# Performance work log

Measured on AMD Instinct MI355X. Metric: run time of the kernel, lower is better.

The kernel has to match this reference:

```python
import jax, jax.numpy as jnp
import numpy as np

N_E = 8192
E_DIM = 256
BETA = 0.25


def setup_inputs() -> dict:
    key = jax.random.key(0)
    k_z, k_w = jax.random.split(key)
    z = jax.random.normal(k_z, (32, E_DIM, 32, 32), dtype=jnp.float32)
    # nn.Embedding weight init: uniform(-1/n_e, 1/n_e)
    W = jax.random.uniform(k_w, (N_E, E_DIM), dtype=jnp.float32,
                           minval=-1.0 / N_E, maxval=1.0 / N_E)
    return {"z": z, "W": W}


def reference(z, W):
    B, C, H, Wd = z.shape
    beta = jnp.float32(BETA)
    z_nhwc = jnp.transpose(z, (0, 2, 3, 1))          # (B,H,W,C)
    zf = z_nhwc.reshape(-1, C)                       # (N,C)
    # squared-distance matrix (N, n_e)
    d = (jnp.sum(zf * zf, axis=1, keepdims=True)
         + jnp.sum(W * W, axis=1)
         - 2.0 * jnp.matmul(zf, W.T))
    idx = jnp.argmin(d, axis=1)                      # (N,)
    # one-hot @ W == gather
    z_q = W[idx].reshape(z_nhwc.shape)               # (B,H,W,C)
    loss = (jnp.mean((jax.lax.stop_gradient(z_q) - z_nhwc) ** 2)
            + beta * jnp.mean((z_q - jax.lax.stop_gradient(z_nhwc)) ** 2))
    # straight-through estimator
    z_q = z_nhwc + jax.lax.stop_gradient(z_q - z_nhwc)
    # codebook usage perplexity
    n = idx.shape[0]
    e_mean = jnp.zeros((N_E,), jnp.float32).at[idx].add(1.0) / n
    perplexity = jnp.exp(-jnp.sum(e_mean * jnp.log(e_mean + 1e-10)))
    z_q = jnp.transpose(z_q, (0, 3, 1, 2))           # back to (B,C,H,W)
    index = idx.reshape(B, H, Wd)
    return z_q, loss, index, perplexity
```

## Files before the change

kernel.cpp:

```cpp
#include <hip/hip_runtime.h>
#include <float.h>
#include <math.h>

#define OUT_LOSS 8388608
#define OUT_IDX  8388609
#define OUT_PERP 8421377

#define WS_ZH    0ull
#define WS_ZL    16777216ull
#define WS_ZT    0ull
#define WS_WH    33554432ull
#define WS_S     37748736ull
#define WS_B     37879808ull
#define WS_MAXW  37912576ull
#define WS_IDX   37912640ull
#define WS_HIST  38043712ull
#define WS_CAND  38076480ull
#define WS_FULL  38469696ull
#define WS_FKEY  38600768ull
#define WS_CNT   38862912ull
#define WS_LOSS  38862920ull
#define WS_WL    38866944ull

typedef short v8s __attribute__((ext_vector_type(8)));
typedef float v4f __attribute__((ext_vector_type(4)));

__device__ __forceinline__ unsigned short bf16rne(float f) {
  unsigned u = __float_as_uint(f);
  return (unsigned short)((u + 0x7FFFu + ((u >> 16) & 1u)) >> 16);
}
__device__ __forceinline__ float bf16tof(unsigned short h) {
  return __uint_as_float(((unsigned)h) << 16);
}

__device__ __forceinline__ void gl_lds16(const void* g, void* l) {
  __builtin_amdgcn_global_load_lds(
      (const __attribute__((address_space(1))) unsigned int*)g,
      (__attribute__((address_space(3))) unsigned int*)l, 16, 0, 0);
}

__global__ void k_zero(int* __restrict__ hist, unsigned long long* __restrict__ fkey,
                       int* __restrict__ cnt, double* __restrict__ loss,
                       unsigned* __restrict__ maxw) {
  const int i = blockIdx.x * 256 + threadIdx.x;
  if (i < 8192) hist[i] = 0;
  else if (i < 40960) fkey[i - 8192] = ~0ull;
  else if (i == 40960) cnt[0] = 0;
  else if (i == 40961) cnt[1] = 0;
  else if (i == 40962) *loss = 0.0;
  else if (i == 40963) *maxw = 0u;
}

__global__ __launch_bounds__(256) void k_split(const float* __restrict__ W,
                                               unsigned short* __restrict__ Wh,
                                               unsigned short* __restrict__ Wl) {
  const int u = blockIdx.x * 256 + threadIdx.x;
  const int kc = u >> 15, grp = (u >> 6) & 511, q = (u >> 4) & 3, col = u & 15;
  const int j = grp * 16 + col, k0 = kc * 32 + q * 8;
  const float4 w0 = *(const float4*)(W + (size_t)j * 256 + k0);
  const float4 w1 = *(const float4*)(W + (size_t)j * 256 + k0 + 4);
  const float wv[8] = {w0.x, w0.y, w0.z, w0.w, w1.x, w1.y, w1.z, w1.w};
  unsigned short h[8] __attribute__((aligned(16)));
  unsigned short l[8] __attribute__((aligned(16)));
#pragma unroll
  for (int i = 0; i < 8; ++i) {
    h[i] = bf16rne(wv[i]);
    l[i] = bf16rne(__fsub_rn(wv[i], bf16tof(h[i])));
  }
  *(uint4*)(Wh + (size_t)u * 8) = *(const uint4*)h;
  *(uint4*)(Wl + (size_t)u * 8) = *(const uint4*)l;
}

__global__ __launch_bounds__(256) void k_splitz(const float* __restrict__ z,
    unsigned short* __restrict__ Zh, unsigned short* __restrict__ Zl) {
  const int gt = blockIdx.x * 256 + threadIdx.x;
  const int kc = gt >> 15;
  const int n  = gt & 32767;
  const int b = n >> 10, p = n & 1023;
  const float* zp = z + (size_t)b * 262144 + (size_t)(kc * 32) * 1024 + p;
  unsigned short hh[32] __attribute__((aligned(16)));
  unsigned short ll[32] __attribute__((aligned(16)));
#pragma unroll
  for (int i = 0; i < 32; ++i) {
    const float v = zp[(size_t)i * 1024];
    const unsigned short h = bf16rne(v);
    hh[i] = h;
    ll[i] = bf16rne(__fsub_rn(v, bf16tof(h)));
  }
  const size_t o = (size_t)kc * 1048576 + (size_t)(n >> 4) * 512 + (size_t)(n & 15) * 8;
#pragma unroll
  for (int q = 0; q < 4; ++q) *(uint4*)(Zh + o + q * 128) = *(const uint4*)(hh + q * 8);
#pragma unroll
  for (int q = 0; q < 4; ++q) *(uint4*)(Zl + o + q * 128) = *(const uint4*)(ll + q * 8);
}

__global__ __launch_bounds__(256) void k_zt(const float* __restrict__ z,
                                            float* __restrict__ zT) {
  const int gt = blockIdx.x * 256 + threadIdx.x;
  const int kc = gt >> 15;
  const int n  = gt & 32767;
  const int b = n >> 10, p = n & 1023;
  const float* zp = z + (size_t)b * 262144 + (size_t)(kc * 32) * 1024 + p;
  float v[32] __attribute__((aligned(16)));
#pragma unroll
  for (int i = 0; i < 32; ++i) v[i] = zp[(size_t)i * 1024];
  float* dst = zT + (size_t)n * 256 + kc * 32;
#pragma unroll
  for (int j = 0; j < 8; ++j) *(float4*)(dst + j * 4) = *(const float4*)(v + j * 4);
}

__device__ __forceinline__ float np_sumsq256(const float* __restrict__ base,
                                             const int stride) {
  float h[2];
#pragma unroll
  for (int half = 0; half < 2; ++half) {
    const float* a = base + (size_t)(half * 128) * stride;
    float r[8];
#pragma unroll
    for (int k = 0; k < 8; ++k) { const float v = a[(size_t)k * stride]; r[k] = __fmul_rn(v, v); }
    for (int i = 8; i < 128; i += 8) {
#pragma unroll
      for (int k = 0; k < 8; ++k) {
        const float v = a[(size_t)(i + k) * stride];
        r[k] = __fadd_rn(r[k], __fmul_rn(v, v));
      }
    }
    h[half] = __fadd_rn(
        __fadd_rn(__fadd_rn(r[0], r[1]), __fadd_rn(r[2], r[3])),
        __fadd_rn(__fadd_rn(r[4], r[5]), __fadd_rn(r[6], r[7])));
  }
  return __fadd_rn(h[0], h[1]);
}

__global__ __launch_bounds__(256) void k_sz(const float* __restrict__ z,
                                            float* __restrict__ S) {
  const int n = blockIdx.x * 256 + threadIdx.x;
  S[n] = np_sumsq256(z + (size_t)(n >> 10) * 262144 + (n & 1023), 1024);
}

__global__ __launch_bounds__(256) void k_wsq(const float* __restrict__ W,
                                             float* __restrict__ B,
                                             unsigned* __restrict__ maxw) {
  const int j = blockIdx.x * 256 + threadIdx.x;
  const float b = np_sumsq256(W + (size_t)j * 256, 1);
  B[j] = b;
  atomicMax(maxw, __float_as_uint(b));
}

__device__ __forceinline__ void merge5(float& a1, int& ai1, float& a2, int& ai2,
                                       float& a3, float b1, int bi1, float b2,
                                       int bi2, float b3) {
  const bool t1 = (b1 < a1) || (b1 == a1 && bi1 < ai1);
  const float w2v = t1 ? b2 : a2; const int w2i = t1 ? bi2 : ai2;
  const float w3v = t1 ? b3 : a3;
  const float l1v = t1 ? a1 : b1; const int l1i = t1 ? ai1 : bi1;
  const float l2v = t1 ? a2 : b2;
  const float n1v = t1 ? b1 : a1; const int n1i = t1 ? bi1 : ai1;
  const bool t2 = (w2v < l1v) || (w2v == l1v && w2i < l1i);
  a1 = n1v; ai1 = n1i;
  a2 = t2 ? w2v : l1v; ai2 = t2 ? w2i : l1i;
  a3 = t2 ? fminf(w3v, l1v) : fminf(w2v, l2v);
}

#define AH_OFF   0
#define AL_OFF   32768
#define B0_OFF   65536
#define B1_OFF   73728
#define SC_OFF   0
#define SMEM_SZ  81920
__global__ __launch_bounds__(256, 2) void k_main(
    const unsigned short* __restrict__ Zh, const unsigned short* __restrict__ Zl,
    const unsigned short* __restrict__ Wh, const unsigned short* __restrict__ Wl,
    const float* __restrict__ S, const float* __restrict__ B,
    const unsigned* __restrict__ maxw, int* __restrict__ idxb,
    int* __restrict__ cand, int* __restrict__ full, int* __restrict__ cnt) {
  extern __shared__ __align__(16) char smem[];
  const int t = threadIdx.x;
  const int w = t >> 6, lane = t & 63, col = lane & 15, q = lane >> 4;
  const int phalf = w >> 1, strip = w & 1;
  const int n0 = blockIdx.x << 6;

  float spx[8];
#pragma unroll
  for (int s = 0; s < 8; ++s)
    spx[s] = S[n0 + phalf * 32 + (s >> 2) * 16 + q * 4 + (s & 3)];

  {
#pragma unroll
    for (int c = 0; c < 2; ++c) {
      const int kc = w * 2 + c;
      const size_t ab = (size_t)kc * 1048576 + (size_t)(n0 >> 4) * 512 + (size_t)lane * 8;
#pragma unroll
      for (int g = 0; g < 4; ++g) {
        gl_lds16(Zh + ab + (size_t)g * 512, smem + AH_OFF + kc * 4096 + g * 1024);
        gl_lds16(Zl + ab + (size_t)g * 512, smem + AL_OFF + kc * 4096 + g * 1024);
      }
    }
  }
  {
    const size_t bb = (size_t)(w * 2) * 512 + (size_t)lane * 8;
    gl_lds16(Wh + bb,       smem + B0_OFF + (w * 2) * 1024);
    gl_lds16(Wh + bb + 512, smem + B0_OFF + (w * 2 + 1) * 1024);
  }
  v8s bl[4];
  {
    const unsigned short* p = Wl + (size_t)(strip * 4) * 512 + (size_t)lane * 8;
#pragma unroll
    for (int nt = 0; nt < 4; ++nt) bl[nt] = *(const v8s*)(p + nt * 512);
  }
  __syncthreads();

  float m1[8], m2[8], m3[8]; int i1[8], i2[8];
#pragma unroll
  for (int s = 0; s < 8; ++s) {
    m1[s] = FLT_MAX; m2[s] = FLT_MAX; m3[s] = FLT_MAX;
    i1[s] = 0x7fffffff; i2[s] = 0x7fffffff;
  }

  v4f acc[2][4];
#pragma unroll
  for (int pt = 0; pt < 2; ++pt)
#pragma unroll
    for (int nt = 0; nt < 4; ++nt) acc[pt][nt] = (v4f){0.f, 0.f, 0.f, 0.f};

  for (int ct = 0; ct < 64; ++ct) {
#pragma unroll
    for (int kc = 0; kc < 8; ++kc) {
      const int it = ct * 8 + kc;
      if (it < 511) {
        const int nc = it + 1;
        const size_t cb = (size_t)(nc & 7) * 262144 + (size_t)(nc >> 3) * 4096
                        + (size_t)(w * 2) * 512 + (size_t)lane * 8;
        char* nh = smem + ((nc & 1) ? B1_OFF : B0_OFF) + (w * 2) * 1024;
        gl_lds16(Wh + cb,       nh);
        gl_lds16(Wh + cb + 512, nh + 1024);
      }
      const char* bhb = smem + ((it & 1) ? B1_OFF : B0_OFF);
      const int nc2 = (it + 1) & 511;
      const unsigned short* blsrc = Wl + (size_t)(nc2 & 7) * 262144
                                  + (size_t)(nc2 >> 3) * 4096
                                  + (size_t)(strip * 4) * 512 + (size_t)lane * 8;
      v8s ah[2], al[2];
#pragma unroll
      for (int pt = 0; pt < 2; ++pt) {
        const int g = phalf * 2 + pt;
        ah[pt] = *(const v8s*)(smem + AH_OFF + kc * 4096 + g * 1024 + lane * 16);
        al[pt] = *(const v8s*)(smem + AL_OFF + kc * 4096 + g * 1024 + lane * 16);
      }
#pragma unroll
      for (int nt = 0; nt < 4; ++nt) {
        const v8s bh = *(const v8s*)(bhb + (strip * 4 + nt) * 1024 + lane * 16);
        const v8s blv = bl[nt];
#pragma unroll
        for (int pt = 0; pt < 2; ++pt) {
          acc[pt][nt] = __builtin_amdgcn_mfma_f32_16x16x32_bf16(ah[pt], bh, acc[pt][nt], 0, 0, 0);
          acc[pt][nt] = __builtin_amdgcn_mfma_f32_16x16x32_bf16(al[pt], bh, acc[pt][nt], 0, 0, 0);
          acc[pt][nt] = __builtin_amdgcn_mfma_f32_16x16x32_bf16(ah[pt], blv, acc[pt][nt], 0, 0, 0);
        }
        bl[nt] = *(const v8s*)(blsrc + nt * 512);
      }
      __syncthreads();
      if (kc == 7) {
#pragma unroll
        for (int nt = 0; nt < 4; ++nt) {
          const int code = ct * 128 + strip * 64 + nt * 16 + col;
          const float bb = B[code];
#pragma unroll
          for (int pt = 0; pt < 2; ++pt) {
            const v4f a = acc[pt][nt];
#pragma unroll
            for (int r = 0; r < 4; ++r) {
              const int s = pt * 4 + r;
              const float d = __fsub_rn(__fadd_rn(spx[s], bb), __fmul_rn(2.f, a[r]));
              const bool c1 = (d < m1[s]);
              const bool c2 = (d < m2[s]);
              const bool c3 = (d < m3[s]);
              m3[s] = c2 ? m2[s] : (c3 ? d : m3[s]);
              m2[s] = c1 ? m1[s] : (c2 ? d : m2[s]);
              i2[s] = c1 ? i1[s] : (c2 ? code : i2[s]);
              m1[s] = c1 ? d : m1[s];
              i1[s] = c1 ? code : i1[s];
            }
          }
#pragma unroll
          for (int pt = 0; pt < 2; ++pt) acc[pt][nt] = (v4f){0.f, 0.f, 0.f, 0.f};
        }
      }
    }
  }

#pragma unroll
  for (int s = 0; s < 8; ++s) {
    for (int msk = 1; msk < 16; msk <<= 1) {
      const float b1 = __shfl_xor(m1[s], msk, 16);
      const int  bi1 = __shfl_xor(i1[s], msk, 16);
      const float b2 = __shfl_xor(m2[s], msk, 16);
      const int  bi2 = __shfl_xor(i2[s], msk, 16);
      const float b3 = __shfl_xor(m3[s], msk, 16);
      merge5(m1[s], i1[s], m2[s], i2[s], m3[s], b1, bi1, b2, bi2, b3);
    }
  }
  __syncthreads();
  float* sc = (float*)(smem + SC_OFF);
  if (col == 0) {
#pragma unroll
    for (int s = 0; s < 8; ++s) {
      const int px = phalf * 32 + (s >> 2) * 16 + q * 4 + (s & 3);
      const int base = (px * 2 + strip) * 5;
      sc[base]     = m1[s];
      sc[base + 1] = __int_as_float(i1[s]);
      sc[base + 2] = m2[s];
      sc[base + 3] = __int_as_float(i2[s]);
      sc[base + 4] = m3[s];
    }
  }
  __syncthreads();
  if (t < 64) {
    const int base0 = t * 10;
    float A1 = sc[base0], A2 = sc[base0 + 2], A3 = sc[base0 + 4];
    int AI1 = __float_as_int(sc[base0 + 1]), AI2 = __float_as_int(sc[base0 + 3]);
    {
      const int base = base0 + 5;
      merge5(A1, AI1, A2, AI2, A3, sc[base], __float_as_int(sc[base + 1]),
             sc[base + 2], __float_as_int(sc[base + 3]), sc[base + 4]);
    }
    const int n = n0 + t;
    idxb[n] = AI1;
    const float nw = sqrtf(S[n]) * sqrtf(__uint_as_float(*maxw));
    const float win = 2.0f * (1.52587890625e-05f * nw + 1e-6f)
                    + 2.0f * ldexpf(1.0f, ilogbf(fmaxf(A1, 1e-30f)) - 23);
    if (A2 <= A1 + win) {
      if (A3 <= A1 + win) {
        const int p = atomicAdd(&cnt[1], 1);
        full[p] = n;
      } else {
        const int p = atomicAdd(&cnt[0], 1);
        cand[3 * p] = n; cand[3 * p + 1] = AI1; cand[3 * p + 2] = AI2;
      }
    }
  }
}

__global__ __launch_bounds__(256) void k_cand(const float* __restrict__ zT,
    const float* __restrict__ W, const float* __restrict__ S,
    const float* __restrict__ B, const int* __restrict__ cand,
    const int* __restrict__ cnt, int* __restrict__ idxb) {
  const int e = blockIdx.x * 256 + threadIdx.x;
  if (e >= cnt[0]) return;
  const int n = cand[3 * e], ca = cand[3 * e + 1], cb = cand[3 * e + 2];
  const float* zp = zT + (size_t)n * 256;
  const float* wa = W + (size_t)ca * 256;
  const float* wb = W + (size_t)cb * 256;
  float a1 = 0.f, a2 = 0.f;
  for (int c = 0; c < 256; ++c) {
    const float zv = zp[c];
    a1 = __builtin_fmaf(zv, wa[c], a1);
    a2 = __builtin_fmaf(zv, wb[c], a2);
  }
  const float d1 = __fsub_rn(__fadd_rn(S[n], B[ca]), __fmul_rn(2.f, a1));
  const float d2 = __fsub_rn(__fadd_rn(S[n], B[cb]), __fmul_rn(2.f, a2));
  idxb[n] = (d1 < d2) ? ca : ((d2 < d1) ? cb : min(ca, cb));
}

__global__ __launch_bounds__(256) void k_full(const float* __restrict__ zT,
    const float* __restrict__ W, const float* __restrict__ S,
    const float* __restrict__ B, const int* __restrict__ full,
    const int* __restrict__ cnt, unsigned long long* __restrict__ fkey) {
  extern __shared__ __align__(16) char fsm[];
  float* zsf = (float*)fsm;
  float* wt  = (float*)(fsm + 32768);
  float* mv  = (float*)(fsm + 32768 + 32896);
  int*   mi  = (int*)(fsm + 32768 + 32896 + 4224);
  const int t = threadIdx.x;
  const int pg = t & 7, cg = t >> 3;
  const int fN = min(cnt[1], 32768);
  const int units = ((fN + 31) >> 5) << 5;
  for (int e = blockIdx.x; e < units; e += 2048) {
    const int g = e >> 5, tt = e & 31;
    const int c0 = tt << 8;
    __syncthreads();
    {
      const int px = t >> 3, c8 = t & 7;
      const int f = (g << 5) + px;
      const int n = (f < fN) ? full[f] : full[0];
      const float4* src = (const float4*)(zT + (size_t)n * 256 + c8 * 32);
      const int colq = (((px >> 2) ^ c8) << 2) + (px & 3);
#pragma unroll
      for (int j = 0; j < 8; ++j) {
        const float4 v = src[j];
        const int c = c8 * 32 + j * 4;
        zsf[(c    ) * 32 + colq] = v.x;
        zsf[(c + 1) * 32 + colq] = v.y;
        zsf[(c + 2) * 32 + colq] = v.z;
        zsf[(c + 3) * 32 + colq] = v.w;
      }
    }
    float s4[4];
#pragma unroll
    for (int i = 0; i < 4; ++i) {
      const int f = (g << 5) + (pg << 2) + i;
      s4[i] = (f < fN) ? S[full[f]] : 0.f;
    }
    float bm[4]; int bj[4];
#pragma unroll
    for (int i = 0; i < 4; ++i) { bm[i] = FLT_MAX; bj[i] = 0x7fffffff; }
    float acc[4][8];
#pragma unroll
    for (int i = 0; i < 4; ++i)
#pragma unroll
      for (int u = 0; u < 8; ++u) acc[i][u] = 0.f;
    for (int kc = 0; kc < 8; ++kc) {
      const int kb = kc << 5;
      __syncthreads();
#pragma unroll
      for (int p = 0; p < 8; ++p) {
        const int jl = (t >> 3) + (p << 5);
        const float4 wv4 =
            *(const float4*)&W[(size_t)(c0 + jl) * 256 + kb + ((t & 7) << 2)];
        const int k0 = (t & 7) << 2;
        wt[(k0    ) * 257 + jl] = wv4.x;
        wt[(k0 + 1) * 257 + jl] = wv4.y;
        wt[(k0 + 2) * 257 + jl] = wv4.z;
        wt[(k0 + 3) * 257 + jl] = wv4.w;
      }
      __syncthreads();
      const int zq = ((pg ^ kc) & 7) << 2;
      for (int k = 0; k < 32; ++k) {
        const float4 z4 = *(const float4*)&zsf[(kb + k) * 32 + zq];
        const float4 wA = *(const float4*)&wt[k * 257 + (cg << 3)];
        const float4 wB = *(const float4*)&wt[k * 257 + (cg << 3) + 4];
        const float zv[4] = {z4.x, z4.y, z4.z, z4.w};
        const float wv[8] = {wA.x, wA.y, wA.z, wA.w, wB.x, wB.y, wB.z, wB.w};
#pragma unroll
        for (int i = 0; i < 4; ++i)
#pragma unroll
          for (int u = 0; u < 8; ++u)
            acc[i][u] = __builtin_fmaf(zv[i], wv[u], acc[i][u]);
      }
    }
#pragma unroll
    for (int u = 0; u < 8; ++u) {
      const int code = c0 + (cg << 3) + u;
      const float bb = B[code];
#pragma unroll
      for (int i = 0; i < 4; ++i) {
        const float d = __fsub_rn(__fadd_rn(s4[i], bb), __fmul_rn(2.f, acc[i][u]));
        if (d < bm[i]) { bm[i] = d; bj[i] = code; }
      }
    }
    __syncthreads();
#pragma unroll
    for (int i = 0; i < 4; ++i) {
      const int px = (pg << 2) + i;
      mv[px * 33 + cg] = bm[i];
      mi[px * 33 + cg] = bj[i];
    }
    __syncthreads();
    if (t < 32) {
      float m = mv[t * 33]; int j = mi[t * 33];
      for (int c = 1; c < 32; ++c) {
        const float v = mv[t * 33 + c]; const int vi = mi[t * 33 + c];
        if (v < m || (v == m && vi < j)) { m = v; j = vi; }
      }
      const int f = (g << 5) + t;
      if (f < fN) {
        const unsigned long long key =
            (((unsigned long long)__float_as_uint(m)) << 13) | (unsigned)j;
        atomicMin(&fkey[f], key);
      }
    }
  }
}

__global__ __launch_bounds__(256) void k_fullfin(const int* __restrict__ full,
    const int* __restrict__ cnt, const unsigned long long* __restrict__ fkey,
    int* __restrict__ idxb) {
  const int f = blockIdx.x * 256 + threadIdx.x;
  if (f < cnt[1]) idxb[full[f]] = (int)(fkey[f] & 8191ull);
}

__global__ __launch_bounds__(256) void k_zq(const float* __restrict__ z,
    const float* __restrict__ W, const int* __restrict__ idxb,
    float* __restrict__ out, double* __restrict__ loss, int* __restrict__ hist) {
  __shared__ float red[256];
  const int t = threadIdx.x;
  const int tx = t & 63, ty = t >> 6;
  const int n0 = blockIdx.x << 6;
  const int n = n0 + tx;
  const int b = n >> 10;
  const int p = n & 1023;
  const int myidx = idxb[n];
  const float* wrow = W + (size_t)myidx * 256;
  float lsum = 0.f;
#pragma unroll 4
  for (int cc = 0; cc < 64; ++cc) {
    const int c = ty * 64 + cc;
    const float qv = wrow[c];
    const size_t off = (size_t)b * 262144 + (size_t)c * 1024 + p;
    const float zv = z[off];
    const float d = __fsub_rn(qv, zv);
    lsum = __builtin_fmaf(d, d, lsum);
    out[off] = __fadd_rn(zv, d);
  }
  red[t] = lsum;
  __syncthreads();
  for (int o = 128; o > 0; o >>= 1) {
    if (t < o) red[t] += red[t + o];
    __syncthreads();
  }
  if (t == 0) atomicAdd(loss, (double)red[0]);
  if (ty == 0) atomicAdd(&hist[myidx], 1);
  if (ty == 1) out[OUT_IDX + n] = (float)myidx;
}

__global__ void k_final(const int* __restrict__ hist,
                        const double* __restrict__ loss,
                        float* __restrict__ out) {
  __shared__ double sh[256];
  const int t = threadIdx.x;
  double s = 0.0;
  for (int j = t; j < 8192; j += 256) {
    const double e = (double)hist[j] / 32768.0;
    s += e * log(e + 1e-10);
  }
  sh[t] = s;
  __syncthreads();
  for (int off = 128; off > 0; off >>= 1) {
    if (t < off) sh[t] += sh[t + off];
    __syncthreads();
  }
  if (t == 0) {
    out[OUT_PERP] = (float)exp(-sh[0]);
    out[OUT_LOSS] = (float)(1.25 * (*loss) / 8388608.0);
  }
}

extern "C" void kernel_launch(void* const* d_in, const int* in_sizes, int n_in,
                              void* d_out, int out_size, void* d_ws, size_t ws_size,
                              hipStream_t stream) {
  const float* z = (const float*)d_in[0];
  const float* W = (const float*)d_in[1];
  float* out = (float*)d_out;
  char* ws = (char*)d_ws;
  unsigned short* Zh = (unsigned short*)(ws + WS_ZH);
  unsigned short* Zl = (unsigned short*)(ws + WS_ZL);
  unsigned short* Wh = (unsigned short*)(ws + WS_WH);
  unsigned short* Wl = (unsigned short*)(ws + WS_WL);
  float*  zT   = (float*)(ws + WS_ZT);
  float*  S    = (float*)(ws + WS_S);
  float*  B    = (float*)(ws + WS_B);
  unsigned* maxw = (unsigned*)(ws + WS_MAXW);
  int*    idxb = (int*)(ws + WS_IDX);
  int*    hist = (int*)(ws + WS_HIST);
  int*    cand = (int*)(ws + WS_CAND);
  int*    full = (int*)(ws + WS_FULL);
  unsigned long long* fkey = (unsigned long long*)(ws + WS_FKEY);
  int*    cnt  = (int*)(ws + WS_CNT);
  double* loss = (double*)(ws + WS_LOSS);

  hipLaunchKernelGGL(k_zero,    dim3(161),  dim3(256), 0, stream, hist, fkey, cnt, loss, maxw);
  hipLaunchKernelGGL(k_split,   dim3(1024), dim3(256), 0, stream, W, Wh, Wl);
  hipLaunchKernelGGL(k_splitz,  dim3(1024), dim3(256), 0, stream, z, Zh, Zl);
  hipLaunchKernelGGL(k_sz,      dim3(128),  dim3(256), 0, stream, z, S);
  hipLaunchKernelGGL(k_wsq,     dim3(32),   dim3(256), 0, stream, W, B, maxw);
  hipLaunchKernelGGL(k_main,    dim3(512),  dim3(256), SMEM_SZ, stream,
                     Zh, Zl, Wh, Wl, S, B, maxw, idxb, cand, full, cnt);
  hipLaunchKernelGGL(k_zt,      dim3(1024), dim3(256), 0, stream, z, zT);
  hipLaunchKernelGGL(k_cand,    dim3(128),  dim3(256), 0, stream, zT, W, S, B, cand, cnt, idxb);
  hipLaunchKernelGGL(k_full,    dim3(2048), dim3(256), 74112, stream, zT, W, S, B, full, cnt, fkey);
  hipLaunchKernelGGL(k_fullfin, dim3(128),  dim3(256), 0, stream, full, cnt, fkey, idxb);
  hipLaunchKernelGGL(k_zq,      dim3(512),  dim3(256), 0, stream, z, W, idxb, out, loss, hist);
  hipLaunchKernelGGL(k_final,   dim3(1),    dim3(256), 0, stream, hist, loss, out);
}
```

Baseline: 739.9 us.

## Load W tiles directly into registers with double-buffering, removing LDS staging and barriers

The inner GEMM loop no longer stages the high half of the codebook in shared memory with a per-iteration __syncthreads. Each wave now loads both the high and low W fragments straight from global memory into two register buffers that alternate, with the loop unrolled by two. This removes LDS traffic and a block-wide barrier from every k-step and cuts shared memory from 80 KB to 64 KB. In exchange, every wave does redundant global/L2 loads of W, since strips no longer share through LDS, and register pressure rises, which could hurt occupancy under launch_bounds(256,2).

```diff
diff --git a/kernel.cpp b/kernel.cpp
--- a/kernel.cpp
+++ b/kernel.cpp
@@ -164,10 +164,8 @@
 
 #define AH_OFF   0
 #define AL_OFF   32768
-#define B0_OFF   65536
-#define B1_OFF   73728
 #define SC_OFF   0
-#define SMEM_SZ  81920
+#define SMEM_SZ  65536
 __global__ __launch_bounds__(256, 2) void k_main(
     const unsigned short* __restrict__ Zh, const unsigned short* __restrict__ Zl,
     const unsigned short* __restrict__ Wh, const unsigned short* __restrict__ Wl,
@@ -197,16 +195,15 @@
       }
     }
   }
-  {
-    const size_t bb = (size_t)(w * 2) * 512 + (size_t)lane * 8;
-    gl_lds16(Wh + bb,       smem + B0_OFF + (w * 2) * 1024);
-    gl_lds16(Wh + bb + 512, smem + B0_OFF + (w * 2 + 1) * 1024);
-  }
-  v8s bl[4];
-  {
-    const unsigned short* p = Wl + (size_t)(strip * 4) * 512 + (size_t)lane * 8;
-#pragma unroll
-    for (int nt = 0; nt < 4; ++nt) bl[nt] = *(const v8s*)(p + nt * 512);
+  const unsigned short* pWh = Wh + (size_t)(strip * 4) * 512 + (size_t)lane * 8;
+  const unsigned short* pWl = Wl + (size_t)(strip * 4) * 512 + (size_t)lane * 8;
+#define BOFF(f) ((size_t)(((f) >> 2) & 7) * 262144 + (size_t)((f) >> 5) * 4096 \
+                 + (size_t)((f) & 3) * 512)
+  v8s bhA[4], blA[4], bhB[4], blB[4];
+#pragma unroll
+  for (int nt = 0; nt < 4; ++nt) {
+    bhA[nt] = *(const v8s*)(pWh + BOFF(nt));
+    blA[nt] = *(const v8s*)(pWl + BOFF(nt));
   }
   __syncthreads();
 
@@ -223,23 +220,16 @@
 #pragma unroll
     for (int nt = 0; nt < 4; ++nt) acc[pt][nt] = (v4f){0.f, 0.f, 0.f, 0.f};
 
-  for (int ct = 0; ct < 64; ++ct) {
-#pragma unroll
-    for (int kc = 0; kc < 8; ++kc) {
-      const int it = ct * 8 + kc;
-      if (it < 511) {
-        const int nc = it + 1;
-        const size_t cb = (size_t)(nc & 7) * 262144 + (size_t)(nc >> 3) * 4096
-                        + (size_t)(w * 2) * 512 + (size_t)lane * 8;
-        char* nh = smem + ((nc & 1) ? B1_OFF : B0_OFF) + (w * 2) * 1024;
-        gl_lds16(Wh + cb,       nh);
-        gl_lds16(Wh + cb + 512, nh + 1024);
-      }
-      const char* bhb = smem + ((it & 1) ? B1_OFF : B0_OFF);
-      const int nc2 = (it + 1) & 511;
-      const unsigned short* blsrc = Wl + (size_t)(nc2 & 7) * 262144
-                                  + (size_t)(nc2 >> 3) * 4096
-                                  + (size_t)(strip * 4) * 512 + (size_t)lane * 8;
+  for (int it2 = 0; it2 < 256; ++it2) {
+    {
+      const int it = it2 * 2;
+      const int kc = it & 7;
+      const int fn = ((it + 1) * 4) & 2047;
+#pragma unroll
+      for (int nt = 0; nt < 4; ++nt) {
+        bhB[nt] = *(const v8s*)(pWh + BOFF(fn + nt));
+        blB[nt] = *(const v8s*)(pWl + BOFF(fn + nt));
+      }
       v8s ah[2], al[2];
 #pragma unroll
       for (int pt = 0; pt < 2; ++pt) {
@@ -249,18 +239,41 @@
       }
 #pragma unroll
       for (int nt = 0; nt < 4; ++nt) {
-        const v8s bh = *(const v8s*)(bhb + (strip * 4 + nt) * 1024 + lane * 16);
-        const v8s blv = bl[nt];
 #pragma unroll
         for (int pt = 0; pt < 2; ++pt) {
-          acc[pt][nt] = __builtin_amdgcn_mfma_f32_16x16x32_bf16(ah[pt], bh, acc[pt][nt], 0, 0, 0);
-          acc[pt][nt] = __builtin_amdgcn_mfma_f32_16x16x32_bf16(al[pt], bh, acc[pt][nt], 0, 0, 0);
-          acc[pt][nt] = __builtin_amdgcn_mfma_f32_16x16x32_bf16(ah[pt], blv, acc[pt][nt], 0, 0, 0);
+          acc[pt][nt] = __builtin_amdgcn_mfma_f32_16x16x32_bf16(ah[pt], bhA[nt], acc[pt][nt], 0, 0, 0);
+          acc[pt][nt] = __builtin_amdgcn_mfma_f32_16x16x32_bf16(al[pt], bhA[nt], acc[pt][nt], 0, 0, 0);
+          acc[pt][nt] = __builtin_amdgcn_mfma_f32_16x16x32_bf16(ah[pt], blA[nt], acc[pt][nt], 0, 0, 0);
         }
-        bl[nt] = *(const v8s*)(blsrc + nt * 512);
-      }
-      __syncthreads();
+      }
+    }
+    {
+      const int it = it2 * 2 + 1;
+      const int kc = it & 7;
+      const int fn = ((it + 1) * 4) & 2047;
+#pragma unroll
+      for (int nt = 0; nt < 4; ++nt) {
+        bhA[nt] = *(const v8s*)(pWh + BOFF(fn + nt));
+        blA[nt] = *(const v8s*)(pWl + BOFF(fn + nt));
+      }
+      v8s ah[2], al[2];
+#pragma unroll
+      for (int pt = 0; pt < 2; ++pt) {
+        const int g = phalf * 2 + pt;
+        ah[pt] = *(const v8s*)(smem + AH_OFF + kc * 4096 + g * 1024 + lane * 16);
+        al[pt] = *(const v8s*)(smem + AL_OFF + kc * 4096 + g * 1024 + lane * 16);
+      }
+#pragma unroll
+      for (int nt = 0; nt < 4; ++nt) {
+#pragma unroll
+        for (int pt = 0; pt < 2; ++pt) {
+          acc[pt][nt] = __builtin_amdgcn_mfma_f32_16x16x32_bf16(ah[pt], bhB[nt], acc[pt][nt], 0, 0, 0);
+          acc[pt][nt] = __builtin_amdgcn_mfma_f32_16x16x32_bf16(al[pt], bhB[nt], acc[pt][nt], 0, 0, 0);
+          acc[pt][nt] = __builtin_amdgcn_mfma_f32_16x16x32_bf16(ah[pt], blB[nt], acc[pt][nt], 0, 0, 0);
+        }
+      }
       if (kc == 7) {
+        const int ct = it >> 3;
 #pragma unroll
         for (int nt = 0; nt < 4; ++nt) {
           const int code = ct * 128 + strip * 64 + nt * 16 + col;
@@ -288,6 +301,7 @@
       }
     }
   }
+#undef BOFF
 
 #pragma unroll
   for (int s = 0; s < 8; ++s) {
```

New measurement: 816.0 us. 10.3% more time.

## Triple-buffer codebook tiles in LDS and keep low-half activations in registers

Applied to the files above, without the earlier changes.

Moves the low-bf16 half of the z tile out of LDS into registers (16 v8s per thread). It replaces the double-buffered Wh tiles with a three-stage LDS ring prefetched two iterations ahead, and double-buffers the Wl register loads. The full __syncthreads is replaced by a partial vmcnt wait plus s_barrier so loads can stay in flight across iterations. This cuts LDS footprint and read traffic and deepens the prefetch, at the cost of many more VGPRs, which could cause spills or lower occupancy under launch_bounds(256,2).

```diff
diff --git a/kernel.cpp b/kernel.cpp
--- a/kernel.cpp
+++ b/kernel.cpp
@@ -163,11 +163,11 @@
 }
 
 #define AH_OFF   0
-#define AL_OFF   32768
-#define B0_OFF   65536
-#define B1_OFF   73728
+#define BH0_OFF  32768
+#define BH1_OFF  40960
+#define BH2_OFF  49152
 #define SC_OFF   0
-#define SMEM_SZ  81920
+#define SMEM_SZ  57344
 __global__ __launch_bounds__(256, 2) void k_main(
     const unsigned short* __restrict__ Zh, const unsigned short* __restrict__ Zl,
     const unsigned short* __restrict__ Wh, const unsigned short* __restrict__ Wl,
@@ -191,24 +191,38 @@
       const int kc = w * 2 + c;
       const size_t ab = (size_t)kc * 1048576 + (size_t)(n0 >> 4) * 512 + (size_t)lane * 8;
 #pragma unroll
-      for (int g = 0; g < 4; ++g) {
+      for (int g = 0; g < 4; ++g)
         gl_lds16(Zh + ab + (size_t)g * 512, smem + AH_OFF + kc * 4096 + g * 1024);
-        gl_lds16(Zl + ab + (size_t)g * 512, smem + AL_OFF + kc * 4096 + g * 1024);
-      }
-    }
-  }
+    }
+  }
+  v8s al[8][2];
   {
-    const size_t bb = (size_t)(w * 2) * 512 + (size_t)lane * 8;
-    gl_lds16(Wh + bb,       smem + B0_OFF + (w * 2) * 1024);
-    gl_lds16(Wh + bb + 512, smem + B0_OFF + (w * 2 + 1) * 1024);
-  }
-  v8s bl[4];
+    const size_t abase = (size_t)(n0 >> 4) * 512 + (size_t)lane * 8;
+#pragma unroll
+    for (int kc = 0; kc < 8; ++kc)
+#pragma unroll
+      for (int pt = 0; pt < 2; ++pt)
+        al[kc][pt] = *(const v8s*)(Zl + (size_t)kc * 1048576 + abase
+                                   + (size_t)(phalf * 2 + pt) * 512);
+  }
+  {
+#pragma unroll
+    for (int c = 0; c < 2; ++c) {
+      const size_t cb = (size_t)c * 262144 + (size_t)(w * 2) * 512 + (size_t)lane * 8;
+      char* d = smem + (c ? BH1_OFF : BH0_OFF) + (w * 2) * 1024;
+      gl_lds16(Wh + cb,       d);
+      gl_lds16(Wh + cb + 512, d + 1024);
+    }
+  }
+  v8s blA[4], blB[4];
   {
     const unsigned short* p = Wl + (size_t)(strip * 4) * 512 + (size_t)lane * 8;
 #pragma unroll
-    for (int nt = 0; nt < 4; ++nt) bl[nt] = *(const v8s*)(p + nt * 512);
-  }
-  __syncthreads();
+    for (int nt = 0; nt < 4; ++nt) blA[nt] = *(const v8s*)(p + nt * 512);
+  }
+  asm volatile("s_waitcnt vmcnt(0)" ::: "memory");
+  __builtin_amdgcn_s_barrier();
+  asm volatile("" ::: "memory");
 
   float m1[8], m2[8], m3[8]; int i1[8], i2[8];
 #pragma unroll
@@ -223,44 +237,53 @@
 #pragma unroll
     for (int nt = 0; nt < 4; ++nt) acc[pt][nt] = (v4f){0.f, 0.f, 0.f, 0.f};
 
-  for (int ct = 0; ct < 64; ++ct) {
+  char* cur = smem + BH0_OFF;
+  char* nxt = smem + BH1_OFF;
+  char* nx2 = smem + BH2_OFF;
+
+  for (int it2 = 0; it2 < 64; ++it2) {
 #pragma unroll
     for (int kc = 0; kc < 8; ++kc) {
-      const int it = ct * 8 + kc;
-      if (it < 511) {
-        const int nc = it + 1;
+      const int it = it2 * 8 + kc;
+      if (it < 510) {
+        const int nc = it + 2;
         const size_t cb = (size_t)(nc & 7) * 262144 + (size_t)(nc >> 3) * 4096
                         + (size_t)(w * 2) * 512 + (size_t)lane * 8;
-        char* nh = smem + ((nc & 1) ? B1_OFF : B0_OFF) + (w * 2) * 1024;
-        gl_lds16(Wh + cb,       nh);
-        gl_lds16(Wh + cb + 512, nh + 1024);
-      }
-      const char* bhb = smem + ((it & 1) ? B1_OFF : B0_OFF);
-      const int nc2 = (it + 1) & 511;
-      const unsigned short* blsrc = Wl + (size_t)(nc2 & 7) * 262144
+        char* d = nx2 + (w * 2) * 1024;
+        gl_lds16(Wh + cb,       d);
+        gl_lds16(Wh + cb + 512, d + 1024);
+      }
+      {
+        const int nc2 = (it + 1) & 511;
+        const unsigned short* bls = Wl + (size_t)(nc2 & 7) * 262144
                                   + (size_t)(nc2 >> 3) * 4096
                                   + (size_t)(strip * 4) * 512 + (size_t)lane * 8;
-      v8s ah[2], al[2];
-#pragma unroll
-      for (int pt = 0; pt < 2; ++pt) {
-        const int g = phalf * 2 + pt;
-        ah[pt] = *(const v8s*)(smem + AH_OFF + kc * 4096 + g * 1024 + lane * 16);
-        al[pt] = *(const v8s*)(smem + AL_OFF + kc * 4096 + g * 1024 + lane * 16);
-      }
+        if ((kc & 1) == 0) {
+#pragma unroll
+          for (int nt = 0; nt < 4; ++nt) blB[nt] = *(const v8s*)(bls + nt * 512);
+        } else {
+#pragma unroll
+          for (int nt = 0; nt < 4; ++nt) blA[nt] = *(const v8s*)(bls + nt * 512);
+        }
+      }
+      v8s ah[2];
+#pragma unroll
+      for (int pt = 0; pt < 2; ++pt)
+        ah[pt] = *(const v8s*)(smem + AH_OFF + kc * 4096
+                               + (phalf * 2 + pt) * 1024 + lane * 16);
 #pragma unroll
       for (int nt = 0; nt < 4; ++nt) {
-        const v8s bh = *(const v8s*)(bhb + (strip * 4 + nt) * 1024 + lane * 16);
-        const v8s blv = bl[nt];
+        const v8s bh = *(const v8s*)(cur + (strip * 4 + nt) * 1024 + lane * 16);
+        const v8s blv = (kc & 1) ? blB[nt] : blA[nt];
 #pragma unroll
         for (int pt = 0; pt < 2; ++pt) {
           acc[pt][nt] = __builtin_amdgcn_mfma_f32_16x16x32_bf16(ah[pt], bh, acc[pt][nt], 0, 0, 0);
-          acc[pt][nt] = __builtin_amdgcn_mfma_f32_16x16x32_bf16(al[pt], bh, acc[pt][nt], 0, 0, 0);
+          acc[pt][nt] = __builtin_amdgcn_mfma_f32_16x16x32_bf16(al[kc][pt], bh, acc[pt][nt], 0, 0, 0);
           acc[pt][nt] = __builtin_amdgcn_mfma_f32_16x16x32_bf16(ah[pt], blv, acc[pt][nt], 0, 0, 0);
         }
-        bl[nt] = *(const v8s*)(blsrc + nt * 512);
-      }
-      __syncthreads();
+      }
       if (kc == 7) {
+        const int ct = it >> 3;
 #pragma unroll
         for (int nt = 0; nt < 4; ++nt) {
           const int code = ct * 128 + strip * 64 + nt * 16 + col;
@@ -286,6 +309,12 @@
           for (int pt = 0; pt < 2; ++pt) acc[pt][nt] = (v4f){0.f, 0.f, 0.f, 0.f};
         }
       }
+      if (it < 511) {
+        asm volatile("s_waitcnt vmcnt(6)" ::: "memory");
+        __builtin_amdgcn_s_barrier();
+        asm volatile("" ::: "memory");
+      }
+      char* tmp = cur; cur = nxt; nxt = nx2; nx2 = tmp;
     }
   }
 
```

Result: faster. 698.0 us (-5.7%).
